# Performance work log

Hardware: AMD Instinct MI355X
Metric: run time of the kernel (lower is better)

Reference implementation:

```python
import jax, jax.numpy as jnp
import numpy as np

B, S, D, H = 8, 1024, 1024, 16
DH = D // H


def setup_inputs() -> dict:
    key = jax.random.key(0)
    ks = jax.random.split(key, 8)
    x = jax.random.normal(ks[0], (B, S, D), dtype=jnp.float32)
    # Whisper-style additive causal mask: -inf above the diagonal
    mask = jnp.triu(jnp.full((S, S), -jnp.inf, dtype=jnp.float32), k=1)
    s = 0.02
    Wq = jax.random.normal(ks[1], (D, D), jnp.float32) * s
    bq = jax.random.normal(ks[2], (D,), jnp.float32) * s
    Wk = jax.random.normal(ks[3], (D, D), jnp.float32) * s
    Wv = jax.random.normal(ks[4], (D, D), jnp.float32) * s
    bv = jax.random.normal(ks[5], (D,), jnp.float32) * s
    Wo = jax.random.normal(ks[6], (D, D), jnp.float32) * s
    bo = jax.random.normal(ks[7], (D,), jnp.float32) * s
    return {"x": x, "mask": mask, "Wq": Wq, "bq": bq, "Wk": Wk, "Wv": Wv,
            "bv": bv, "Wo": Wo, "bo": bo}


def reference(x, mask, Wq, bq, Wk, Wv, bv, Wo, bo):
    n_head = H
    d_head = D // n_head
    scale = d_head ** -0.25

    # Projections (torch Linear: y = x @ W.T + b; key has no bias)
    q = x @ Wq.T + bq           # [B,S,D]
    k = x @ Wk.T                # [B,S,D]
    v = x @ Wv.T + bv           # [B,S,D]

    # [B,S,D] -> [B,H,S,dh]
    q = q.reshape(B, S, n_head, d_head).transpose(0, 2, 1, 3)
    k = k.reshape(B, S, n_head, d_head).transpose(0, 2, 1, 3)
    v = v.reshape(B, S, n_head, d_head).transpose(0, 2, 1, 3)

    # Manual (non-fused) attention, fp32 softmax, as in the torch path
    qk = jnp.einsum('bhqd,bhkd->bhqk', q * scale, k * scale)
    qk = qk + mask[:S, :S]
    qk = qk.astype(jnp.float32)
    w = jax.nn.softmax(qk, axis=-1).astype(q.dtype)
    out = jnp.einsum('bhqk,bhkd->bhqd', w, v)
    out = out.transpose(0, 2, 1, 3).reshape(B, S, D)
    out = out @ Wo.T + bo
    qk = jax.lax.stop_gradient(qk)
    return out, qk
```

## Files before the change

### kernel.cpp

```cpp
#include <hip/hip_runtime.h>
#include <math.h>

constexpr int B_ = 8, S_ = 1024, D_ = 1024, H_ = 16, DH_ = 64;
constexpr float SCALE2 = 0.125f;
constexpr float MASK_NEG = -1e30f;

typedef __attribute__((ext_vector_type(8))) short short8;
typedef __attribute__((ext_vector_type(4))) float f32x4;

union S8U { short8 s8; unsigned u[4]; };

__device__ __forceinline__ void cvt_split_store(short* hi, short* lo, float4 v) {
  unsigned u0 = __float_as_uint(v.x), u1 = __float_as_uint(v.y);
  unsigned u2 = __float_as_uint(v.z), u3 = __float_as_uint(v.w);
  unsigned h0 = u0 & 0xFFFF0000u, h1 = u1 & 0xFFFF0000u;
  unsigned h2 = u2 & 0xFFFF0000u, h3 = u3 & 0xFFFF0000u;
  float l0 = v.x - __uint_as_float(h0);
  float l1 = v.y - __uint_as_float(h1);
  float l2 = v.z - __uint_as_float(h2);
  float l3 = v.w - __uint_as_float(h3);
  uint2 hp = make_uint2(h1 | (h0 >> 16), h3 | (h2 >> 16));
  unsigned w0 = __float_as_uint(l0), w1 = __float_as_uint(l1);
  unsigned w2 = __float_as_uint(l2), w3 = __float_as_uint(l3);
  uint2 lp = make_uint2((w1 & 0xFFFF0000u) | (w0 >> 16),
                        (w3 & 0xFFFF0000u) | (w2 >> 16));
  *(uint2*)hi = hp;
  *(uint2*)lo = lp;
}

__device__ __forceinline__ void cvt8(const float* f, short8* hi, short8* lo) {
  S8U h, l;
#pragma unroll
  for (int i = 0; i < 4; ++i) {
    float a = f[2 * i], b = f[2 * i + 1];
    unsigned ua = __float_as_uint(a), ub = __float_as_uint(b);
    unsigned ha = ua & 0xFFFF0000u, hb = ub & 0xFFFF0000u;
    float la = a - __uint_as_float(ha);
    float lb = b - __uint_as_float(hb);
    h.u[i] = hb | (ha >> 16);
    l.u[i] = (__float_as_uint(lb) & 0xFFFF0000u) | (__float_as_uint(la) >> 16);
  }
  *hi = h.s8;
  *lo = l.s8;
}

__device__ __forceinline__ unsigned pack_sp(float f) {
  unsigned u = __float_as_uint(f);
  unsigned hb = u & 0xFFFF0000u;
  float lo = f - __uint_as_float(hb);
  return hb | (__float_as_uint(lo) >> 16);
}

__device__ __forceinline__ void unpack8(uint4 a, uint4 b, short8* hi, short8* lo) {
  S8U h, l;
  h.u[0] = (a.y & 0xFFFF0000u) | (a.x >> 16);
  h.u[1] = (a.w & 0xFFFF0000u) | (a.z >> 16);
  h.u[2] = (b.y & 0xFFFF0000u) | (b.x >> 16);
  h.u[3] = (b.w & 0xFFFF0000u) | (b.z >> 16);
  l.u[0] = (a.y << 16) | (a.x & 0xFFFFu);
  l.u[1] = (a.w << 16) | (a.z & 0xFFFFu);
  l.u[2] = (b.y << 16) | (b.x & 0xFFFFu);
  l.u[3] = (b.w << 16) | (b.z & 0xFFFFu);
  *hi = h.s8;
  *lo = l.s8;
}

template <bool VT>
__global__ __launch_bounds__(256) void gemm_nt_mfma(
    const float* __restrict__ A, const float* __restrict__ W,
    const float* __restrict__ bias, float* __restrict__ C,
    int M, int N, int K) {
  __shared__ __align__(16) short A_hi[128][40];
  __shared__ __align__(16) short A_lo[128][40];
  __shared__ __align__(16) short B_hi[128][40];
  __shared__ __align__(16) short B_lo[128][40];

  const int tid = threadIdx.x;
  const int m0 = blockIdx.y * 128, n0 = blockIdx.x * 128;
  const int wave = tid >> 6, lane = tid & 63;
  const int wm = (wave & 1) * 64, wn = (wave >> 1) * 64;
  const int lm = lane & 15;
  const int koff = (lane >> 4) * 8;

  const int srow = tid >> 3;
  const int sc4 = (tid & 7) * 4;

  f32x4 acc[4][4];
#pragma unroll
  for (int i = 0; i < 4; ++i)
#pragma unroll
    for (int j = 0; j < 4; ++j) acc[i][j] = (f32x4){0.f, 0.f, 0.f, 0.f};

  for (int k0 = 0; k0 < K; k0 += 32) {
    __syncthreads();
#pragma unroll
    for (int pass = 0; pass < 4; ++pass) {
      const int r = srow + pass * 32;
      float4 av = *(const float4*)(A + (size_t)(m0 + r) * K + k0 + sc4);
      float4 wv = *(const float4*)(W + (size_t)(n0 + r) * K + k0 + sc4);
      cvt_split_store(&A_hi[r][sc4], &A_lo[r][sc4], av);
      cvt_split_store(&B_hi[r][sc4], &B_lo[r][sc4], wv);
    }
    __syncthreads();

    short8 ah[4], al[4], bh[4], bl[4];
#pragma unroll
    for (int i = 0; i < 4; ++i) {
      ah[i] = *(const short8*)&A_hi[wm + i * 16 + lm][koff];
      al[i] = *(const short8*)&A_lo[wm + i * 16 + lm][koff];
      bh[i] = *(const short8*)&B_hi[wn + i * 16 + lm][koff];
      bl[i] = *(const short8*)&B_lo[wn + i * 16 + lm][koff];
    }
#pragma unroll
    for (int i = 0; i < 4; ++i)
#pragma unroll
      for (int j = 0; j < 4; ++j) {
        acc[i][j] = __builtin_amdgcn_mfma_f32_16x16x32_bf16(ah[i], bh[j], acc[i][j], 0, 0, 0);
        acc[i][j] = __builtin_amdgcn_mfma_f32_16x16x32_bf16(ah[i], bl[j], acc[i][j], 0, 0, 0);
        acc[i][j] = __builtin_amdgcn_mfma_f32_16x16x32_bf16(al[i], bh[j], acc[i][j], 0, 0, 0);
      }
  }

  const int crow0 = (lane >> 4) * 4;
  const int ccol = lane & 15;
#pragma unroll
  for (int i = 0; i < 4; ++i) {
    const int m = m0 + wm + i * 16 + crow0;
#pragma unroll
    for (int j = 0; j < 4; ++j) {
      const int n = n0 + wn + j * 16 + ccol;
      const float bv_ = bias ? bias[n] : 0.f;
      if (VT) {
        const int bb = m >> 10, ss = m & 1023;
        float4 t = make_float4(acc[i][j][0] + bv_, acc[i][j][1] + bv_,
                               acc[i][j][2] + bv_, acc[i][j][3] + bv_);
        *(float4*)(C + ((size_t)bb * D_ + n) * S_ + ss) = t;
      } else {
#pragma unroll
        for (int r = 0; r < 4; ++r)
          C[(size_t)(m + r) * N + n] = acc[i][j][r] + bv_;
      }
    }
  }
}

__global__ __launch_bounds__(256) void attn_fused(
    const float* __restrict__ q, const float* __restrict__ k,
    const float* __restrict__ vT, float* __restrict__ qk,
    float* __restrict__ attn) {
  __shared__ __align__(16) short K_hi[64][72];
  __shared__ __align__(16) short K_lo[64][72];
  __shared__ __align__(16) short V_hi[64][72];
  __shared__ __align__(16) short V_lo[64][72];
  __shared__ __align__(16) unsigned P_p[64][68];

  const int it = blockIdx.x;
  const int bh = blockIdx.y;
  const int b = bh >> 4, h = bh & 15;
  const int tid = threadIdx.x;
  const int wave = tid >> 6, lane = tid & 63;
  const int lm = lane & 15, lg = lane >> 4;
  const int wq = wave * 16;
  const int koff = lg * 8;
  const int crow0 = lg * 4;
  const int sr = tid >> 4;
  const int sc = (tid & 15) * 4;

  short8 qh[2], ql[2];
  {
    const float* qp = q + ((size_t)(b * S_ + it * 64 + wq + lm)) * D_ + h * DH_;
#pragma unroll
    for (int kc = 0; kc < 2; ++kc) {
      float4 x0 = *(const float4*)(qp + kc * 32 + koff);
      float4 x1 = *(const float4*)(qp + kc * 32 + koff + 4);
      float f[8] = {x0.x * SCALE2, x0.y * SCALE2, x0.z * SCALE2, x0.w * SCALE2,
                    x1.x * SCALE2, x1.y * SCALE2, x1.z * SCALE2, x1.w * SCALE2};
      cvt8(f, &qh[kc], &ql[kc]);
    }
  }

  f32x4 O[4];
#pragma unroll
  for (int i = 0; i < 4; ++i) O[i] = (f32x4){0.f, 0.f, 0.f, 0.f};
  f32x4 mreg = (f32x4){MASK_NEG, MASK_NEG, MASK_NEG, MASK_NEG};
  f32x4 lreg = (f32x4){0.f, 0.f, 0.f, 0.f};

  float* qkrow = qk + ((size_t)bh << 20) + (size_t)it * 64 * S_;

  for (int jt = 0; jt <= it; ++jt) {
    __syncthreads();
#pragma unroll
    for (int p = 0; p < 4; ++p) {
      const int r = p * 16 + sr;
      float4 kv = *(const float4*)(k + ((size_t)(b * S_ + jt * 64 + r)) * D_ + h * DH_ + sc);
      float4 vv = *(const float4*)(vT + ((size_t)(b * D_ + h * DH_ + r)) * S_ + jt * 64 + sc);
      cvt_split_store(&K_hi[r][sc], &K_lo[r][sc], kv);
      cvt_split_store(&V_hi[r][sc], &V_lo[r][sc], vv);
    }
    __syncthreads();

    f32x4 sacc[4];
#pragma unroll
    for (int j4 = 0; j4 < 4; ++j4) sacc[j4] = (f32x4){0.f, 0.f, 0.f, 0.f};
#pragma unroll
    for (int kc = 0; kc < 2; ++kc)
#pragma unroll
      for (int j4 = 0; j4 < 4; ++j4) {
        short8 kh = *(const short8*)&K_hi[j4 * 16 + lm][kc * 32 + koff];
        short8 kl = *(const short8*)&K_lo[j4 * 16 + lm][kc * 32 + koff];
        sacc[j4] = __builtin_amdgcn_mfma_f32_16x16x32_bf16(qh[kc], kh, sacc[j4], 0, 0, 0);
        sacc[j4] = __builtin_amdgcn_mfma_f32_16x16x32_bf16(qh[kc], kl, sacc[j4], 0, 0, 0);
        sacc[j4] = __builtin_amdgcn_mfma_f32_16x16x32_bf16(ql[kc], kh, sacc[j4], 0, 0, 0);
      }

    if (jt == it) {
#pragma unroll
      for (int j4 = 0; j4 < 4; ++j4)
#pragma unroll
        for (int r = 0; r < 4; ++r)
          if (j4 * 16 + lm > wq + crow0 + r) sacc[j4][r] = MASK_NEG;
    }

#pragma unroll
    for (int j4 = 0; j4 < 4; ++j4)
#pragma unroll
      for (int r = 0; r < 4; ++r)
        qkrow[(size_t)(wq + crow0 + r) * S_ + jt * 64 + j4 * 16 + lm] = sacc[j4][r];

    f32x4 tmax = sacc[0];
#pragma unroll
    for (int j4 = 1; j4 < 4; ++j4)
#pragma unroll
      for (int r = 0; r < 4; ++r) tmax[r] = fmaxf(tmax[r], sacc[j4][r]);
#pragma unroll
    for (int off = 1; off < 16; off <<= 1)
#pragma unroll
      for (int r = 0; r < 4; ++r) tmax[r] = fmaxf(tmax[r], __shfl_xor(tmax[r], off));

    f32x4 fac, mnew;
#pragma unroll
    for (int r = 0; r < 4; ++r) {
      mnew[r] = fmaxf(mreg[r], tmax[r]);
      fac[r] = __expf(mreg[r] - mnew[r]);
      mreg[r] = mnew[r];
    }
    f32x4 tsum = (f32x4){0.f, 0.f, 0.f, 0.f};
#pragma unroll
    for (int j4 = 0; j4 < 4; ++j4)
#pragma unroll
      for (int r = 0; r < 4; ++r) {
        float pv = __expf(sacc[j4][r] - mnew[r]);
        sacc[j4][r] = pv;
        tsum[r] += pv;
      }
#pragma unroll
    for (int off = 1; off < 16; off <<= 1)
#pragma unroll
      for (int r = 0; r < 4; ++r) tsum[r] += __shfl_xor(tsum[r], off);
#pragma unroll
    for (int r = 0; r < 4; ++r) lreg[r] = lreg[r] * fac[r] + tsum[r];
#pragma unroll
    for (int d4 = 0; d4 < 4; ++d4)
#pragma unroll
      for (int r = 0; r < 4; ++r) O[d4][r] *= fac[r];

#pragma unroll
    for (int j4 = 0; j4 < 4; ++j4)
#pragma unroll
      for (int r = 0; r < 4; ++r)
        P_p[wq + crow0 + r][j4 * 16 + lm] = pack_sp(sacc[j4][r]);
    __syncthreads();

#pragma unroll
    for (int kc = 0; kc < 2; ++kc) {
      const unsigned* pp = &P_p[wq + lm][kc * 32 + koff];
      uint4 a0 = *(const uint4*)pp;
      uint4 a1 = *(const uint4*)(pp + 4);
      short8 ph, pl;
      unpack8(a0, a1, &ph, &pl);
#pragma unroll
      for (int d4 = 0; d4 < 4; ++d4) {
        short8 vh = *(const short8*)&V_hi[d4 * 16 + lm][kc * 32 + koff];
        short8 vl = *(const short8*)&V_lo[d4 * 16 + lm][kc * 32 + koff];
        O[d4] = __builtin_amdgcn_mfma_f32_16x16x32_bf16(ph, vh, O[d4], 0, 0, 0);
        O[d4] = __builtin_amdgcn_mfma_f32_16x16x32_bf16(ph, vl, O[d4], 0, 0, 0);
        O[d4] = __builtin_amdgcn_mfma_f32_16x16x32_bf16(pl, vh, O[d4], 0, 0, 0);
      }
    }
  }

  {
    f32x4 inv;
#pragma unroll
    for (int r = 0; r < 4; ++r) inv[r] = 1.f / lreg[r];
    float* ap = attn + ((size_t)(b * S_ + it * 64 + wq + crow0)) * D_ + h * DH_;
#pragma unroll
    for (int d4 = 0; d4 < 4; ++d4)
#pragma unroll
      for (int r = 0; r < 4; ++r)
        ap[(size_t)r * D_ + d4 * 16 + lm] = O[d4][r] * inv[r];
  }

  const float4 nf = make_float4(MASK_NEG, MASK_NEG, MASK_NEG, MASK_NEG);
  for (int jt = it + 1; jt < 16; ++jt) {
#pragma unroll
    for (int p = 0; p < 4; ++p) {
      const int r = p * 16 + sr;
      *(float4*)(qkrow + (size_t)r * S_ + jt * 64 + sc) = nf;
    }
  }
}

extern "C" void kernel_launch(void* const* d_in, const int* in_sizes, int n_in,
                              void* d_out, int out_size, void* d_ws,
                              size_t ws_size, hipStream_t stream) {
  const float* x  = (const float*)d_in[0];
  const float* Wq = (const float*)d_in[2];
  const float* bq = (const float*)d_in[3];
  const float* Wk = (const float*)d_in[4];
  const float* Wv = (const float*)d_in[5];
  const float* bv = (const float*)d_in[6];
  const float* Wo = (const float*)d_in[7];
  const float* bo = (const float*)d_in[8];

  float* out = (float*)d_out;
  float* qk  = (float*)d_out + (size_t)B_ * S_ * D_;

  float* qbuf  = (float*)d_ws;
  float* kbuf  = qbuf + (size_t)B_ * S_ * D_;
  float* vtbuf = kbuf + (size_t)B_ * S_ * D_;
  float* abuf  = vtbuf + (size_t)B_ * S_ * D_;

  const dim3 gg(D_ / 128, (B_ * S_) / 128);
  gemm_nt_mfma<false><<<gg, 256, 0, stream>>>(x, Wq, bq, qbuf, B_ * S_, D_, D_);
  gemm_nt_mfma<false><<<gg, 256, 0, stream>>>(x, Wk, nullptr, kbuf, B_ * S_, D_, D_);
  gemm_nt_mfma<true><<<gg, 256, 0, stream>>>(x, Wv, bv, vtbuf, B_ * S_, D_, D_);

  attn_fused<<<dim3(16, B_ * H_), 256, 0, stream>>>(qbuf, kbuf, vtbuf, qk, abuf);

  gemm_nt_mfma<false><<<gg, 256, 0, stream>>>(abuf, Wo, bo, out, B_ * S_, D_, D_);
}
```

Baseline: 1.002 ms.

## Pre-split fp32 operands into bf16 hi/lo planes once and feed GEMMs/attention directly

Adds a split_planes kernel that converts x and all four weight matrices into separate bf16 high and low planes once per call. The projection GEMMs now store Q, K and V^T as bf16 hi/lo planes, with the Q scale folded into the epilogue, and the attention kernel writes its output as planes too. This removes the repeated per-tile fp32-to-bf16 splitting inside every GEMM and attention K/V tile load, and replaces fp32 loads with short8 loads. The cost is an extra conversion pass over x and the weights, and a workspace that now holds ten activation-sized short planes.

```diff
diff --git a/kernel.cpp b/kernel.cpp
--- a/kernel.cpp
+++ b/kernel.cpp
@@ -2,7 +2,6 @@
 #include <math.h>
 
 constexpr int B_ = 8, S_ = 1024, D_ = 1024, H_ = 16, DH_ = 64;
-constexpr float SCALE2 = 0.125f;
 constexpr float MASK_NEG = -1e30f;
 
 typedef __attribute__((ext_vector_type(8))) short short8;
@@ -10,38 +9,29 @@
 
 union S8U { short8 s8; unsigned u[4]; };
 
-__device__ __forceinline__ void cvt_split_store(short* hi, short* lo, float4 v) {
-  unsigned u0 = __float_as_uint(v.x), u1 = __float_as_uint(v.y);
-  unsigned u2 = __float_as_uint(v.z), u3 = __float_as_uint(v.w);
-  unsigned h0 = u0 & 0xFFFF0000u, h1 = u1 & 0xFFFF0000u;
-  unsigned h2 = u2 & 0xFFFF0000u, h3 = u3 & 0xFFFF0000u;
-  float l0 = v.x - __uint_as_float(h0);
-  float l1 = v.y - __uint_as_float(h1);
-  float l2 = v.z - __uint_as_float(h2);
-  float l3 = v.w - __uint_as_float(h3);
-  uint2 hp = make_uint2(h1 | (h0 >> 16), h3 | (h2 >> 16));
-  unsigned w0 = __float_as_uint(l0), w1 = __float_as_uint(l1);
-  unsigned w2 = __float_as_uint(l2), w3 = __float_as_uint(l3);
-  uint2 lp = make_uint2((w1 & 0xFFFF0000u) | (w0 >> 16),
-                        (w3 & 0xFFFF0000u) | (w2 >> 16));
-  *(uint2*)hi = hp;
-  *(uint2*)lo = lp;
-}
-
-__device__ __forceinline__ void cvt8(const float* f, short8* hi, short8* lo) {
+__device__ __forceinline__ void split8(float4 a, float4 b, short8* hi, short8* lo) {
+  float f[8] = {a.x, a.y, a.z, a.w, b.x, b.y, b.z, b.w};
   S8U h, l;
 #pragma unroll
   for (int i = 0; i < 4; ++i) {
-    float a = f[2 * i], b = f[2 * i + 1];
-    unsigned ua = __float_as_uint(a), ub = __float_as_uint(b);
-    unsigned ha = ua & 0xFFFF0000u, hb = ub & 0xFFFF0000u;
-    float la = a - __uint_as_float(ha);
-    float lb = b - __uint_as_float(hb);
-    h.u[i] = hb | (ha >> 16);
-    l.u[i] = (__float_as_uint(lb) & 0xFFFF0000u) | (__float_as_uint(la) >> 16);
+    float p = f[2 * i], q = f[2 * i + 1];
+    unsigned up = __float_as_uint(p), uq = __float_as_uint(q);
+    unsigned hp = up & 0xFFFF0000u, hq = uq & 0xFFFF0000u;
+    float lp = p - __uint_as_float(hp);
+    float lq = q - __uint_as_float(hq);
+    h.u[i] = hq | (hp >> 16);
+    l.u[i] = (__float_as_uint(lq) & 0xFFFF0000u) | (__float_as_uint(lp) >> 16);
   }
   *hi = h.s8;
   *lo = l.s8;
+}
+
+__device__ __forceinline__ void split1v(float f, short& hi, short& lo) {
+  unsigned u = __float_as_uint(f);
+  unsigned hb = u & 0xFFFF0000u;
+  float l = f - __uint_as_float(hb);
+  hi = (short)(hb >> 16);
+  lo = (short)(__float_as_uint(l) >> 16);
 }
 
 __device__ __forceinline__ unsigned pack_sp(float f) {
@@ -65,15 +55,40 @@
   *lo = l.s8;
 }
 
-template <bool VT>
-__global__ __launch_bounds__(256) void gemm_nt_mfma(
-    const float* __restrict__ A, const float* __restrict__ W,
-    const float* __restrict__ bias, float* __restrict__ C,
+__global__ __launch_bounds__(256) void split_planes(
+    const float* __restrict__ x, short* xh, short* xl,
+    const float* __restrict__ w0, short* w0h, short* w0l,
+    const float* __restrict__ w1, short* w1h, short* w1l,
+    const float* __restrict__ w2, short* w2h, short* w2l,
+    const float* __restrict__ w3, short* w3h, short* w3l) {
+  const float* src; short *dh, *dl; int n8;
+  switch (blockIdx.y) {
+    case 0:  src = x;  dh = xh;  dl = xl;  n8 = (B_ * S_ * D_) / 8; break;
+    case 1:  src = w0; dh = w0h; dl = w0l; n8 = (D_ * D_) / 8; break;
+    case 2:  src = w1; dh = w1h; dl = w1l; n8 = (D_ * D_) / 8; break;
+    case 3:  src = w2; dh = w2h; dl = w2l; n8 = (D_ * D_) / 8; break;
+    default: src = w3; dh = w3h; dl = w3l; n8 = (D_ * D_) / 8; break;
+  }
+  for (int i = blockIdx.x * 256 + threadIdx.x; i < n8; i += gridDim.x * 256) {
+    float4 a = ((const float4*)src)[2 * i];
+    float4 b = ((const float4*)src)[2 * i + 1];
+    short8 h, l;
+    split8(a, b, &h, &l);
+    ((short8*)dh)[i] = h;
+    ((short8*)dl)[i] = l;
+  }
+}
+
+__global__ __launch_bounds__(256) void gemm_planes(
+    const short* __restrict__ Ah, const short* __restrict__ Al,
+    const short* __restrict__ Wh, const short* __restrict__ Wl,
+    const float* __restrict__ bias, float scale, int mode,
+    float* __restrict__ C, short* __restrict__ Ch, short* __restrict__ Cl,
     int M, int N, int K) {
-  __shared__ __align__(16) short A_hi[128][40];
-  __shared__ __align__(16) short A_lo[128][40];
-  __shared__ __align__(16) short B_hi[128][40];
-  __shared__ __align__(16) short B_lo[128][40];
+  __shared__ __align__(16) short As_h[128][40];
+  __shared__ __align__(16) short As_l[128][40];
+  __shared__ __align__(16) short Bs_h[128][40];
+  __shared__ __align__(16) short Bs_l[128][40];
 
   const int tid = threadIdx.x;
   const int m0 = blockIdx.y * 128, n0 = blockIdx.x * 128;
@@ -82,8 +97,8 @@
   const int lm = lane & 15;
   const int koff = (lane >> 4) * 8;
 
-  const int srow = tid >> 3;
-  const int sc4 = (tid & 7) * 4;
+  const int r0 = tid >> 2, r1 = (tid >> 2) + 64;
+  const int u0 = (tid & 3) * 8;
 
   f32x4 acc[4][4];
 #pragma unroll
@@ -93,23 +108,31 @@
 
   for (int k0 = 0; k0 < K; k0 += 32) {
     __syncthreads();
-#pragma unroll
-    for (int pass = 0; pass < 4; ++pass) {
-      const int r = srow + pass * 32;
-      float4 av = *(const float4*)(A + (size_t)(m0 + r) * K + k0 + sc4);
-      float4 wv = *(const float4*)(W + (size_t)(n0 + r) * K + k0 + sc4);
-      cvt_split_store(&A_hi[r][sc4], &A_lo[r][sc4], av);
-      cvt_split_store(&B_hi[r][sc4], &B_lo[r][sc4], wv);
-    }
+    short8 t0 = *(const short8*)(Ah + (size_t)(m0 + r0) * K + k0 + u0);
+    short8 t1 = *(const short8*)(Ah + (size_t)(m0 + r1) * K + k0 + u0);
+    short8 t2 = *(const short8*)(Al + (size_t)(m0 + r0) * K + k0 + u0);
+    short8 t3 = *(const short8*)(Al + (size_t)(m0 + r1) * K + k0 + u0);
+    short8 t4 = *(const short8*)(Wh + (size_t)(n0 + r0) * K + k0 + u0);
+    short8 t5 = *(const short8*)(Wh + (size_t)(n0 + r1) * K + k0 + u0);
+    short8 t6 = *(const short8*)(Wl + (size_t)(n0 + r0) * K + k0 + u0);
+    short8 t7 = *(const short8*)(Wl + (size_t)(n0 + r1) * K + k0 + u0);
+    *(short8*)&As_h[r0][u0] = t0;
+    *(short8*)&As_h[r1][u0] = t1;
+    *(short8*)&As_l[r0][u0] = t2;
+    *(short8*)&As_l[r1][u0] = t3;
+    *(short8*)&Bs_h[r0][u0] = t4;
+    *(short8*)&Bs_h[r1][u0] = t5;
+    *(short8*)&Bs_l[r0][u0] = t6;
+    *(short8*)&Bs_l[r1][u0] = t7;
     __syncthreads();
 
     short8 ah[4], al[4], bh[4], bl[4];
 #pragma unroll
     for (int i = 0; i < 4; ++i) {
-      ah[i] = *(const short8*)&A_hi[wm + i * 16 + lm][koff];
-      al[i] = *(const short8*)&A_lo[wm + i * 16 + lm][koff];
-      bh[i] = *(const short8*)&B_hi[wn + i * 16 + lm][koff];
-      bl[i] = *(const short8*)&B_lo[wn + i * 16 + lm][koff];
+      ah[i] = *(const short8*)&As_h[wm + i * 16 + lm][koff];
+      al[i] = *(const short8*)&As_l[wm + i * 16 + lm][koff];
+      bh[i] = *(const short8*)&Bs_h[wn + i * 16 + lm][koff];
+      bl[i] = *(const short8*)&Bs_l[wn + i * 16 + lm][koff];
     }
 #pragma unroll
     for (int i = 0; i < 4; ++i)
@@ -130,24 +153,38 @@
     for (int j = 0; j < 4; ++j) {
       const int n = n0 + wn + j * 16 + ccol;
       const float bv_ = bias ? bias[n] : 0.f;
-      if (VT) {
-        const int bb = m >> 10, ss = m & 1023;
-        float4 t = make_float4(acc[i][j][0] + bv_, acc[i][j][1] + bv_,
-                               acc[i][j][2] + bv_, acc[i][j][3] + bv_);
-        *(float4*)(C + ((size_t)bb * D_ + n) * S_ + ss) = t;
-      } else {
+      if (mode == 0) {
 #pragma unroll
         for (int r = 0; r < 4; ++r)
           C[(size_t)(m + r) * N + n] = acc[i][j][r] + bv_;
+      } else if (mode == 1) {
+#pragma unroll
+        for (int r = 0; r < 4; ++r) {
+          float v = (acc[i][j][r] + bv_) * scale;
+          short hv, lv;
+          split1v(v, hv, lv);
+          Ch[(size_t)(m + r) * N + n] = hv;
+          Cl[(size_t)(m + r) * N + n] = lv;
+        }
+      } else {
+        const int bb = m >> 10, ss = m & 1023;
+        short4 hv, lv;
+        split1v(acc[i][j][0] + bv_, hv.x, lv.x);
+        split1v(acc[i][j][1] + bv_, hv.y, lv.y);
+        split1v(acc[i][j][2] + bv_, hv.z, lv.z);
+        split1v(acc[i][j][3] + bv_, hv.w, lv.w);
+        *(short4*)(Ch + ((size_t)bb * D_ + n) * S_ + ss) = hv;
+        *(short4*)(Cl + ((size_t)bb * D_ + n) * S_ + ss) = lv;
       }
     }
   }
 }
 
 __global__ __launch_bounds__(256) void attn_fused(
-    const float* __restrict__ q, const float* __restrict__ k,
-    const float* __restrict__ vT, float* __restrict__ qk,
-    float* __restrict__ attn) {
+    const short* __restrict__ qsh, const short* __restrict__ qsl,
+    const short* __restrict__ ksh, const short* __restrict__ ksl,
+    const short* __restrict__ vsh, const short* __restrict__ vsl,
+    float* __restrict__ qk, short* __restrict__ oh, short* __restrict__ ol) {
   __shared__ __align__(16) short K_hi[64][72];
   __shared__ __align__(16) short K_lo[64][72];
   __shared__ __align__(16) short V_hi[64][72];
@@ -163,20 +200,16 @@
   const int wq = wave * 16;
   const int koff = lg * 8;
   const int crow0 = lg * 4;
-  const int sr = tid >> 4;
-  const int sc = (tid & 15) * 4;
-
-  short8 qh[2], ql[2];
+  const int sr0 = tid >> 3, sr1 = (tid >> 3) + 32;
+  const int sc0 = (tid & 7) * 8;
+
+  short8 qfh[2], qfl[2];
   {
-    const float* qp = q + ((size_t)(b * S_ + it * 64 + wq + lm)) * D_ + h * DH_;
-#pragma unroll
-    for (int kc = 0; kc < 2; ++kc) {
-      float4 x0 = *(const float4*)(qp + kc * 32 + koff);
-      float4 x1 = *(const float4*)(qp + kc * 32 + koff + 4);
-      float f[8] = {x0.x * SCALE2, x0.y * SCALE2, x0.z * SCALE2, x0.w * SCALE2,
-                    x1.x * SCALE2, x1.y * SCALE2, x1.z * SCALE2, x1.w * SCALE2};
-      cvt8(f, &qh[kc], &ql[kc]);
-    }
+    const size_t qb = ((size_t)(b * S_ + it * 64 + wq + lm)) * D_ + h * DH_;
+    qfh[0] = *(const short8*)(qsh + qb + koff);
+    qfh[1] = *(const short8*)(qsh + qb + 32 + koff);
+    qfl[0] = *(const short8*)(qsl + qb + koff);
+    qfl[1] = *(const short8*)(qsl + qb + 32 + koff);
   }
 
   f32x4 O[4];
@@ -189,14 +222,24 @@
 
   for (int jt = 0; jt <= it; ++jt) {
     __syncthreads();
-#pragma unroll
-    for (int p = 0; p < 4; ++p) {
-      const int r = p * 16 + sr;
-      float4 kv = *(const float4*)(k + ((size_t)(b * S_ + jt * 64 + r)) * D_ + h * DH_ + sc);
-      float4 vv = *(const float4*)(vT + ((size_t)(b * D_ + h * DH_ + r)) * S_ + jt * 64 + sc);
-      cvt_split_store(&K_hi[r][sc], &K_lo[r][sc], kv);
-      cvt_split_store(&V_hi[r][sc], &V_lo[r][sc], vv);
-    }
+    const size_t kb = ((size_t)(b * S_ + jt * 64)) * D_ + h * DH_;
+    const size_t vb = ((size_t)(b * D_ + h * DH_)) * S_ + jt * 64;
+    short8 a0 = *(const short8*)(ksh + kb + (size_t)sr0 * D_ + sc0);
+    short8 a1 = *(const short8*)(ksh + kb + (size_t)sr1 * D_ + sc0);
+    short8 a2 = *(const short8*)(ksl + kb + (size_t)sr0 * D_ + sc0);
+    short8 a3 = *(const short8*)(ksl + kb + (size_t)sr1 * D_ + sc0);
+    short8 a4 = *(const short8*)(vsh + vb + (size_t)sr0 * S_ + sc0);
+    short8 a5 = *(const short8*)(vsh + vb + (size_t)sr1 * S_ + sc0);
+    short8 a6 = *(const short8*)(vsl + vb + (size_t)sr0 * S_ + sc0);
+    short8 a7 = *(const short8*)(vsl + vb + (size_t)sr1 * S_ + sc0);
+    *(short8*)&K_hi[sr0][sc0] = a0;
+    *(short8*)&K_hi[sr1][sc0] = a1;
+    *(short8*)&K_lo[sr0][sc0] = a2;
+    *(short8*)&K_lo[sr1][sc0] = a3;
+    *(short8*)&V_hi[sr0][sc0] = a4;
+    *(short8*)&V_hi[sr1][sc0] = a5;
+    *(short8*)&V_lo[sr0][sc0] = a6;
+    *(short8*)&V_lo[sr1][sc0] = a7;
     __syncthreads();
 
     f32x4 sacc[4];
@@ -208,9 +251,9 @@
       for (int j4 = 0; j4 < 4; ++j4) {
         short8 kh = *(const short8*)&K_hi[j4 * 16 + lm][kc * 32 + koff];
         short8 kl = *(const short8*)&K_lo[j4 * 16 + lm][kc * 32 + koff];
-        sacc[j4] = __builtin_amdgcn_mfma_f32_16x16x32_bf16(qh[kc], kh, sacc[j4], 0, 0, 0);
-        sacc[j4] = __builtin_amdgcn_mfma_f32_16x16x32_bf16(qh[kc], kl, sacc[j4], 0, 0, 0);
-        sacc[j4] = __builtin_amdgcn_mfma_f32_16x16x32_bf16(ql[kc], kh, sacc[j4], 0, 0, 0);
+        sacc[j4] = __builtin_amdgcn_mfma_f32_16x16x32_bf16(qfh[kc], kh, sacc[j4], 0, 0, 0);
+        sacc[j4] = __builtin_amdgcn_mfma_f32_16x16x32_bf16(qfh[kc], kl, sacc[j4], 0, 0, 0);
+        sacc[j4] = __builtin_amdgcn_mfma_f32_16x16x32_bf16(qfl[kc], kh, sacc[j4], 0, 0, 0);
       }
 
     if (jt == it) {
@@ -274,10 +317,10 @@
 #pragma unroll
     for (int kc = 0; kc < 2; ++kc) {
       const unsigned* pp = &P_p[wq + lm][kc * 32 + koff];
-      uint4 a0 = *(const uint4*)pp;
-      uint4 a1 = *(const uint4*)(pp + 4);
+      uint4 a0p = *(const uint4*)pp;
+      uint4 a1p = *(const uint4*)(pp + 4);
       short8 ph, pl;
-      unpack8(a0, a1, &ph, &pl);
+      unpack8(a0p, a1p, &ph, &pl);
 #pragma unroll
       for (int d4 = 0; d4 < 4; ++d4) {
         short8 vh = *(const short8*)&V_hi[d4 * 16 + lm][kc * 32 + koff];
@@ -293,20 +336,26 @@
     f32x4 inv;
 #pragma unroll
     for (int r = 0; r < 4; ++r) inv[r] = 1.f / lreg[r];
-    float* ap = attn + ((size_t)(b * S_ + it * 64 + wq + crow0)) * D_ + h * DH_;
+    const size_t ob = ((size_t)(b * S_ + it * 64 + wq + crow0)) * D_ + h * DH_;
 #pragma unroll
     for (int d4 = 0; d4 < 4; ++d4)
 #pragma unroll
-      for (int r = 0; r < 4; ++r)
-        ap[(size_t)r * D_ + d4 * 16 + lm] = O[d4][r] * inv[r];
-  }
-
+      for (int r = 0; r < 4; ++r) {
+        float v = O[d4][r] * inv[r];
+        short hv, lv;
+        split1v(v, hv, lv);
+        oh[ob + (size_t)r * D_ + d4 * 16 + lm] = hv;
+        ol[ob + (size_t)r * D_ + d4 * 16 + lm] = lv;
+      }
+  }
+
+  const int fr = tid >> 4, fc = (tid & 15) * 4;
   const float4 nf = make_float4(MASK_NEG, MASK_NEG, MASK_NEG, MASK_NEG);
   for (int jt = it + 1; jt < 16; ++jt) {
 #pragma unroll
     for (int p = 0; p < 4; ++p) {
-      const int r = p * 16 + sr;
-      *(float4*)(qkrow + (size_t)r * S_ + jt * 64 + sc) = nf;
+      const int r = p * 16 + fr;
+      *(float4*)(qkrow + (size_t)r * S_ + jt * 64 + fc) = nf;
     }
   }
 }
@@ -326,17 +375,38 @@
   float* out = (float*)d_out;
   float* qk  = (float*)d_out + (size_t)B_ * S_ * D_;
 
-  float* qbuf  = (float*)d_ws;
-  float* kbuf  = qbuf + (size_t)B_ * S_ * D_;
-  float* vtbuf = kbuf + (size_t)B_ * S_ * D_;
-  float* abuf  = vtbuf + (size_t)B_ * S_ * D_;
+  const size_t NSD = (size_t)B_ * S_ * D_;
+  const size_t DD = (size_t)D_ * D_;
+  short* p = (short*)d_ws;
+  short* qh = p;   p += NSD;
+  short* ql = p;   p += NSD;
+  short* kh = p;   p += NSD;
+  short* kl = p;   p += NSD;
+  short* vth = p;  p += NSD;
+  short* vtl = p;  p += NSD;
+  short* ah = p;   p += NSD;
+  short* al = p;   p += NSD;
+  short* xh = p;   p += NSD;
+  short* xl = p;   p += NSD;
+  short* wqh = p;  p += DD;  short* wql = p;  p += DD;
+  short* wkh = p;  p += DD;  short* wkl = p;  p += DD;
+  short* wvh = p;  p += DD;  short* wvl = p;  p += DD;
+  short* woh = p;  p += DD;  short* wol = p;  p += DD;
+
+  split_planes<<<dim3(512, 5), 256, 0, stream>>>(
+      x, xh, xl, Wq, wqh, wql, Wk, wkh, wkl, Wv, wvh, wvl, Wo, woh, wol);
 
   const dim3 gg(D_ / 128, (B_ * S_) / 128);
-  gemm_nt_mfma<false><<<gg, 256, 0, stream>>>(x, Wq, bq, qbuf, B_ * S_, D_, D_);
-  gemm_nt_mfma<false><<<gg, 256, 0, stream>>>(x, Wk, nullptr, kbuf, B_ * S_, D_, D_);
-  gemm_nt_mfma<true><<<gg, 256, 0, stream>>>(x, Wv, bv, vtbuf, B_ * S_, D_, D_);
-
-  attn_fused<<<dim3(16, B_ * H_), 256, 0, stream>>>(qbuf, kbuf, vtbuf, qk, abuf);
-
-  gemm_nt_mfma<false><<<gg, 256, 0, stream>>>(abuf, Wo, bo, out, B_ * S_, D_, D_);
-}
+  gemm_planes<<<gg, 256, 0, stream>>>(xh, xl, wqh, wql, bq, 0.125f, 1,
+                                      nullptr, qh, ql, B_ * S_, D_, D_);
+  gemm_planes<<<gg, 256, 0, stream>>>(xh, xl, wkh, wkl, nullptr, 1.f, 1,
+                                      nullptr, kh, kl, B_ * S_, D_, D_);
+  gemm_planes<<<gg, 256, 0, stream>>>(xh, xl, wvh, wvl, bv, 1.f, 2,
+                                      nullptr, vth, vtl, B_ * S_, D_, D_);
+
+  attn_fused<<<dim3(16, B_ * H_), 256, 0, stream>>>(qh, ql, kh, kl, vth, vtl,
+                                                    qk, ah, al);
+
+  gemm_planes<<<gg, 256, 0, stream>>>(ah, al, woh, wol, bo, 1.f, 0,
+                                      out, nullptr, nullptr, B_ * S_, D_, D_);
+}
```

Measured after the change: 1.026 ms. 2.4% more time.
